# Optimization experiments

Hardware: AMD Instinct MI355X
Metric: run time of the kernel (lower is better)

Reference implementation:

```python
import jax, jax.numpy as jnp
import numpy as np

LN_EPS = 1e-5
LEAKY_SLOPE = 0.01


def setup_inputs() -> dict:
    key = jax.random.key(0)
    k1, k2, k3 = jax.random.split(key, 3)
    n, d, ns = 200000, 512, 1024
    x = jax.random.normal(k1, (n, d), dtype=jnp.float32)
    # Kaiming-ish scale for the projection weight [3d, d]
    W = jax.random.normal(k2, (3 * d, d), dtype=jnp.float32) * (1.0 / np.sqrt(3 * d))
    b = jnp.zeros((d,), dtype=jnp.float32)
    gamma = jnp.ones((d,), dtype=jnp.float32)
    beta = jnp.zeros((d,), dtype=jnp.float32)
    batch = jnp.sort(jax.random.randint(k3, (n,), 0, ns, dtype=jnp.int32))
    return {"x": x, "W": W, "b": b, "gamma": gamma, "beta": beta,
            "batch": batch, "num_segments": ns}


def _pool_mean_max_std(x, batch, num_segments):
    # single-pass style segment reductions: sum, sum-of-squares, count, max
    n = x.shape[0]
    count = jax.ops.segment_sum(jnp.ones((n,), x.dtype), batch, num_segments)  # [S]
    s = jax.ops.segment_sum(x, batch, num_segments)                            # [S,d]
    sq = jax.ops.segment_sum(x * x, batch, num_segments)                       # [S,d]
    cnt = jnp.maximum(count, 1.0)[:, None]
    mean = s / cnt                                                             # global_mean_pool
    # masked dense amax == segment max; empty segments -> finfo.min (NEG fill)
    NEG = jnp.finfo(x.dtype).min
    xmax = jax.ops.segment_max(x, batch, num_segments)
    xmax = jnp.where(jnp.isfinite(xmax), xmax, NEG)
    # scatter_std, unbiased=True, divisor clamped to >= 1 (torch_scatter semantics)
    var = (sq - mean * s) / jnp.maximum(count - 1.0, 1.0)[:, None]
    var = jnp.maximum(var, 0.0)
    safe = jnp.where(var > 0, var, 1.0)
    std = jnp.where(var > 0, jnp.sqrt(safe), 0.0)
    return jnp.concatenate([mean, xmax, std], axis=-1)  # [S, 3d]


def reference(x, W, b, gamma, beta, batch, num_segments):
    pooled = _pool_mean_max_std(x, batch, num_segments)        # [S, 3d]
    h = pooled @ W + b                                          # Linear
    mu = jnp.mean(h, axis=-1, keepdims=True)                    # LayerNorm (eps=1e-5)
    v = jnp.mean((h - mu) ** 2, axis=-1, keepdims=True)
    h = (h - mu) / jnp.sqrt(v + LN_EPS) * gamma + beta
    return jnp.where(h >= 0, h, LEAKY_SLOPE * h)                # LeakyReLU
```

## Files before the change

kernel.cpp:

```cpp
#include <hip/hip_runtime.h>
#include <math.h>

#define D 512
#define K3D 1536
#define NEGF (-3.40282346638528859812e+38f)

typedef __bf16 bf16x8 __attribute__((ext_vector_type(8)));
typedef unsigned short ushort8v __attribute__((ext_vector_type(8)));
typedef float f32x4 __attribute__((ext_vector_type(4)));

__device__ __forceinline__ unsigned short f2bf(float f) {
    unsigned int u = __float_as_uint(f);
    unsigned int r = (u + 0x7FFFu + ((u >> 16) & 1u)) >> 16;
    return (unsigned short)r;
}

__device__ __forceinline__ int lower_bound_dev(const int* __restrict__ b, int n, int v) {
    int lo = 0, hi = n;
    while (lo < hi) {
        int mid = (lo + hi) >> 1;
        if (b[mid] < v) lo = mid + 1; else hi = mid;
    }
    return lo;
}

__device__ __forceinline__ void acc4(float4& s, float4& q, float4& m, const float4 v) {
    s.x += v.x; s.y += v.y; s.z += v.z; s.w += v.w;
    q.x = fmaf(v.x, v.x, q.x); q.y = fmaf(v.y, v.y, q.y);
    q.z = fmaf(v.z, v.z, q.z); q.w = fmaf(v.w, v.w, q.w);
    m.x = fmaxf(m.x, v.x); m.y = fmaxf(m.y, v.y);
    m.z = fmaxf(m.z, v.z); m.w = fmaxf(m.w, v.w);
}

__global__ __launch_bounds__(512) void pool_kernel(
    const float* __restrict__ x, const int* __restrict__ batch,
    unsigned short* __restrict__ pooled_b, int n) {
    const int s   = blockIdx.x;
    const int col = threadIdx.x & 127;
    const int rg  = threadIdx.x >> 7;
    const int start = lower_bound_dev(batch, n, s);
    const int end   = lower_bound_dev(batch, n, s + 1);

    const float4* __restrict__ xv = (const float4*)x;

    float4 sum = {0.f, 0.f, 0.f, 0.f};
    float4 sq  = {0.f, 0.f, 0.f, 0.f};
    float4 mx  = {-INFINITY, -INFINITY, -INFINITY, -INFINITY};

    int i = start + rg;
    for (; i + 12 < end; i += 16) {
        float4 v0 = xv[(size_t)(i + 0)  * 128 + col];
        float4 v1 = xv[(size_t)(i + 4)  * 128 + col];
        float4 v2 = xv[(size_t)(i + 8)  * 128 + col];
        float4 v3 = xv[(size_t)(i + 12) * 128 + col];
        acc4(sum, sq, mx, v0);
        acc4(sum, sq, mx, v1);
        acc4(sum, sq, mx, v2);
        acc4(sum, sq, mx, v3);
    }
    for (; i < end; i += 4) {
        float4 v0 = xv[(size_t)i * 128 + col];
        acc4(sum, sq, mx, v0);
    }

    __shared__ __align__(16) float4 red[9 * 128];
    if (rg > 0) {
        const int base = (rg - 1) * 384;
        red[base + col]       = sum;
        red[base + 128 + col] = sq;
        red[base + 256 + col] = mx;
    }
    __syncthreads();
    if (rg == 0) {
#pragma unroll
        for (int g = 0; g < 3; ++g) {
            const int base = g * 384;
            float4 s2 = red[base + col];
            float4 q2 = red[base + 128 + col];
            float4 m2 = red[base + 256 + col];
            sum.x += s2.x; sum.y += s2.y; sum.z += s2.z; sum.w += s2.w;
            sq.x  += q2.x; sq.y  += q2.y; sq.z  += q2.z; sq.w  += q2.w;
            mx.x = fmaxf(mx.x, m2.x); mx.y = fmaxf(mx.y, m2.y);
            mx.z = fmaxf(mx.z, m2.z); mx.w = fmaxf(mx.w, m2.w);
        }

        const float cnt  = (float)(end - start);
        const float inv  = 1.f / fmaxf(cnt, 1.f);
        const float dinv = 1.f / fmaxf(cnt - 1.f, 1.f);

        float4 mean, stdv;
        mean.x = sum.x * inv; mean.y = sum.y * inv;
        mean.z = sum.z * inv; mean.w = sum.w * inv;

        float vx = (sq.x - mean.x * sum.x) * dinv;
        float vy = (sq.y - mean.y * sum.y) * dinv;
        float vz = (sq.z - mean.z * sum.z) * dinv;
        float vw = (sq.w - mean.w * sum.w) * dinv;
        vx = fmaxf(vx, 0.f); vy = fmaxf(vy, 0.f);
        vz = fmaxf(vz, 0.f); vw = fmaxf(vw, 0.f);
        stdv.x = vx > 0.f ? sqrtf(vx) : 0.f;
        stdv.y = vy > 0.f ? sqrtf(vy) : 0.f;
        stdv.z = vz > 0.f ? sqrtf(vz) : 0.f;
        stdv.w = vw > 0.f ? sqrtf(vw) : 0.f;

        float mxx = isfinite(mx.x) ? mx.x : NEGF;
        float mxy = isfinite(mx.y) ? mx.y : NEGF;
        float mxz = isfinite(mx.z) ? mx.z : NEGF;
        float mxw = isfinite(mx.w) ? mx.w : NEGF;

        unsigned short* prow = pooled_b + (size_t)s * K3D;
        ushort4 om = { f2bf(mean.x), f2bf(mean.y), f2bf(mean.z), f2bf(mean.w) };
        ushort4 ox = { f2bf(mxx),    f2bf(mxy),    f2bf(mxz),    f2bf(mxw)    };
        ushort4 os = { f2bf(stdv.x), f2bf(stdv.y), f2bf(stdv.z), f2bf(stdv.w) };
        *(ushort4*)&prow[4 * col]        = om;
        *(ushort4*)&prow[512 + 4 * col]  = ox;
        *(ushort4*)&prow[1024 + 4 * col] = os;
    }
}

__global__ __launch_bounds__(256) void wconv_kernel(
    const float* __restrict__ W, unsigned short* __restrict__ Wt) {
    __shared__ float tile[32][33];
    const int c0 = blockIdx.x * 32;
    const int r0 = blockIdx.y * 32;
    const int t = threadIdx.x;
    const int r = t >> 3, c4 = (t & 7) * 4;
    float4 v = *(const float4*)&W[(size_t)(r0 + r) * D + c0 + c4];
    tile[r][c4 + 0] = v.x; tile[r][c4 + 1] = v.y;
    tile[r][c4 + 2] = v.z; tile[r][c4 + 3] = v.w;
    __syncthreads();
    const int nn = t >> 3, k4 = (t & 7) * 4;
    ushort4 o = { f2bf(tile[k4 + 0][nn]), f2bf(tile[k4 + 1][nn]),
                  f2bf(tile[k4 + 2][nn]), f2bf(tile[k4 + 3][nn]) };
    *(ushort4*)&Wt[(size_t)(c0 + nn) * K3D + r0 + k4] = o;
}

#define GBM 64
#define GBN 64
#define GBK 64
#define LDT 88
#define GSPLIT 4
#define GKC (K3D / GSPLIT)

__global__ __launch_bounds__(256) void mfma_gemm(
    const unsigned short* __restrict__ A,
    const unsigned short* __restrict__ B,
    float* __restrict__ Hp, int S) {
    __shared__ unsigned short As[GBM * LDT];
    __shared__ unsigned short Bs[GBN * LDT];

    const int tid  = threadIdx.x;
    const int wave = tid >> 6;
    const int lane = tid & 63;
    const int m0 = blockIdx.y * GBM;
    const int n0 = blockIdx.x * GBN;
    const int kb = blockIdx.z * GKC;
    const int wm = (wave & 1) * 32;
    const int wn = (wave >> 1) * 32;

    const int sr = tid >> 3;
    const int sc = (tid & 7) * 8;

    const int frow = lane & 15;
    const int fk   = (lane >> 4) * 8;

    f32x4 acc00 = {0.f, 0.f, 0.f, 0.f};
    f32x4 acc01 = {0.f, 0.f, 0.f, 0.f};
    f32x4 acc10 = {0.f, 0.f, 0.f, 0.f};
    f32x4 acc11 = {0.f, 0.f, 0.f, 0.f};

    for (int k0 = kb; k0 < kb + GKC; k0 += GBK) {
        ushort8v a0 = *(const ushort8v*)&A[(size_t)(m0 + sr)      * K3D + k0 + sc];
        ushort8v a1 = *(const ushort8v*)&A[(size_t)(m0 + sr + 32) * K3D + k0 + sc];
        ushort8v b0 = *(const ushort8v*)&B[(size_t)(n0 + sr)      * K3D + k0 + sc];
        ushort8v b1 = *(const ushort8v*)&B[(size_t)(n0 + sr + 32) * K3D + k0 + sc];
        __syncthreads();
        *(ushort8v*)&As[(sr)      * LDT + sc] = a0;
        *(ushort8v*)&As[(sr + 32) * LDT + sc] = a1;
        *(ushort8v*)&Bs[(sr)      * LDT + sc] = b0;
        *(ushort8v*)&Bs[(sr + 32) * LDT + sc] = b1;
        __syncthreads();

#pragma unroll
        for (int ks = 0; ks < GBK; ks += 32) {
            bf16x8 af0 = *(const bf16x8*)&As[(wm + frow)      * LDT + ks + fk];
            bf16x8 af1 = *(const bf16x8*)&As[(wm + 16 + frow) * LDT + ks + fk];
            bf16x8 bv0 = *(const bf16x8*)&Bs[(wn + frow)      * LDT + ks + fk];
            bf16x8 bv1 = *(const bf16x8*)&Bs[(wn + 16 + frow) * LDT + ks + fk];
            acc00 = __builtin_amdgcn_mfma_f32_16x16x32_bf16(af0, bv0, acc00, 0, 0, 0);
            acc01 = __builtin_amdgcn_mfma_f32_16x16x32_bf16(af0, bv1, acc01, 0, 0, 0);
            acc10 = __builtin_amdgcn_mfma_f32_16x16x32_bf16(af1, bv0, acc10, 0, 0, 0);
            acc11 = __builtin_amdgcn_mfma_f32_16x16x32_bf16(af1, bv1, acc11, 0, 0, 0);
        }
    }

    float* out = Hp + (size_t)blockIdx.z * S * D;
    const int orow = (lane >> 4) * 4;
    const int ocol = lane & 15;
#pragma unroll
    for (int r = 0; r < 4; ++r) {
        out[(size_t)(m0 + wm +      orow + r) * D + n0 + wn +      ocol] = acc00[r];
        out[(size_t)(m0 + wm +      orow + r) * D + n0 + wn + 16 + ocol] = acc01[r];
        out[(size_t)(m0 + wm + 16 + orow + r) * D + n0 + wn +      ocol] = acc10[r];
        out[(size_t)(m0 + wm + 16 + orow + r) * D + n0 + wn + 16 + ocol] = acc11[r];
    }
}

__global__ __launch_bounds__(128) void ln_kernel(
    const float* __restrict__ Hp, const float* __restrict__ bias,
    const float* __restrict__ gamma, const float* __restrict__ beta,
    float* __restrict__ out, int S) {
    const int row = blockIdx.x;
    const int tid = threadIdx.x;
    const size_t idx = (size_t)row * 128 + tid;
    const size_t stride = (size_t)S * 128;

    const float4* hp = (const float4*)Hp;
    float4 v0 = hp[idx];
    float4 v1 = hp[idx + stride];
    float4 v2 = hp[idx + 2 * stride];
    float4 v3 = hp[idx + 3 * stride];
    float4 bb = *(const float4*)&bias[4 * tid];
    float4 v;
    v.x = (v0.x + v1.x) + (v2.x + v3.x) + bb.x;
    v.y = (v0.y + v1.y) + (v2.y + v3.y) + bb.y;
    v.z = (v0.z + v1.z) + (v2.z + v3.z) + bb.z;
    v.w = (v0.w + v1.w) + (v2.w + v3.w) + bb.w;

    float s = v.x + v.y + v.z + v.w;
    float q = v.x * v.x + v.y * v.y + v.z * v.z + v.w * v.w;
#pragma unroll
    for (int off = 32; off > 0; off >>= 1) {
        s += __shfl_down(s, off);
        q += __shfl_down(q, off);
    }
    __shared__ float ls[2], lq[2];
    const int wave = tid >> 6, lane = tid & 63;
    if (lane == 0) { ls[wave] = s; lq[wave] = q; }
    __syncthreads();
    s = ls[0] + ls[1];
    q = lq[0] + lq[1];

    const float mu = s * (1.f / 512.f);
    float var = q * (1.f / 512.f) - mu * mu;
    var = fmaxf(var, 0.f);
    const float r = rsqrtf(var + 1e-5f);

    float4 g  = *(const float4*)&gamma[4 * tid];
    float4 bt = *(const float4*)&beta[4 * tid];
    float4 o;
    o.x = (v.x - mu) * r * g.x + bt.x;
    o.y = (v.y - mu) * r * g.y + bt.y;
    o.z = (v.z - mu) * r * g.z + bt.z;
    o.w = (v.w - mu) * r * g.w + bt.w;
    o.x = o.x >= 0.f ? o.x : 0.01f * o.x;
    o.y = o.y >= 0.f ? o.y : 0.01f * o.y;
    o.z = o.z >= 0.f ? o.z : 0.01f * o.z;
    o.w = o.w >= 0.f ? o.w : 0.01f * o.w;
    *(float4*)&out[(size_t)row * D + 4 * tid] = o;
}

extern "C" void kernel_launch(void* const* d_in, const int* in_sizes, int n_in,
                              void* d_out, int out_size, void* d_ws, size_t ws_size,
                              hipStream_t stream) {
    const float* x     = (const float*)d_in[0];
    const float* W     = (const float*)d_in[1];
    const float* b     = (const float*)d_in[2];
    const float* gamma = (const float*)d_in[3];
    const float* beta  = (const float*)d_in[4];
    const int*   batch = (const int*)d_in[5];
    const int n = in_sizes[5];
    const int S = out_size / D;

    char* ws = (char*)d_ws;
    unsigned short* pooled_b = (unsigned short*)ws;
    unsigned short* Wt       = (unsigned short*)(ws + (size_t)S * K3D * 2);
    float*          Hp       = (float*)(ws + (size_t)S * K3D * 2 + (size_t)D * K3D * 2);
    float* out = (float*)d_out;

    pool_kernel<<<S, 512, 0, stream>>>(x, batch, pooled_b, n);
    dim3 gw(D / 32, K3D / 32);
    wconv_kernel<<<gw, 256, 0, stream>>>(W, Wt);
    dim3 gg(D / GBN, S / GBM, GSPLIT);
    mfma_gemm<<<gg, 256, 0, stream>>>(pooled_b, Wt, Hp, S);
    ln_kernel<<<S, 128, 0, stream>>>(Hp, b, gamma, beta, out, S);
}
```

Baseline: 560.0 us.

## Fuse pooling with weight conversion and precompute segment bounds separately

Segment boundaries move into a small bounds kernel, so each pool block no longer runs two binary searches over the batch array. The pooling and W transpose/bf16 conversion are merged into one launch, with the extra blocks handling 64x32 weight tiles, removing one kernel launch and letting the two jobs overlap. Loads of x now use nontemporal hints to avoid polluting cache with streaming data. The cost is an extra small kernel launch and a larger shared-memory footprint per block from the added tile array.

```diff
diff --git a/kernel.cpp b/kernel.cpp
--- a/kernel.cpp
+++ b/kernel.cpp
@@ -24,115 +24,113 @@
     return lo;
 }
 
-__device__ __forceinline__ void acc4(float4& s, float4& q, float4& m, const float4 v) {
-    s.x += v.x; s.y += v.y; s.z += v.z; s.w += v.w;
-    q.x = fmaf(v.x, v.x, q.x); q.y = fmaf(v.y, v.y, q.y);
-    q.z = fmaf(v.z, v.z, q.z); q.w = fmaf(v.w, v.w, q.w);
-    m.x = fmaxf(m.x, v.x); m.y = fmaxf(m.y, v.y);
-    m.z = fmaxf(m.z, v.z); m.w = fmaxf(m.w, v.w);
-}
-
-__global__ __launch_bounds__(512) void pool_kernel(
-    const float* __restrict__ x, const int* __restrict__ batch,
-    unsigned short* __restrict__ pooled_b, int n) {
-    const int s   = blockIdx.x;
-    const int col = threadIdx.x & 127;
-    const int rg  = threadIdx.x >> 7;
-    const int start = lower_bound_dev(batch, n, s);
-    const int end   = lower_bound_dev(batch, n, s + 1);
-
-    const float4* __restrict__ xv = (const float4*)x;
-
-    float4 sum = {0.f, 0.f, 0.f, 0.f};
-    float4 sq  = {0.f, 0.f, 0.f, 0.f};
-    float4 mx  = {-INFINITY, -INFINITY, -INFINITY, -INFINITY};
-
-    int i = start + rg;
-    for (; i + 12 < end; i += 16) {
-        float4 v0 = xv[(size_t)(i + 0)  * 128 + col];
-        float4 v1 = xv[(size_t)(i + 4)  * 128 + col];
-        float4 v2 = xv[(size_t)(i + 8)  * 128 + col];
-        float4 v3 = xv[(size_t)(i + 12) * 128 + col];
-        acc4(sum, sq, mx, v0);
-        acc4(sum, sq, mx, v1);
-        acc4(sum, sq, mx, v2);
-        acc4(sum, sq, mx, v3);
-    }
-    for (; i < end; i += 4) {
-        float4 v0 = xv[(size_t)i * 128 + col];
-        acc4(sum, sq, mx, v0);
-    }
-
-    __shared__ __align__(16) float4 red[9 * 128];
-    if (rg > 0) {
-        const int base = (rg - 1) * 384;
-        red[base + col]       = sum;
-        red[base + 128 + col] = sq;
-        red[base + 256 + col] = mx;
-    }
-    __syncthreads();
-    if (rg == 0) {
-#pragma unroll
-        for (int g = 0; g < 3; ++g) {
-            const int base = g * 384;
-            float4 s2 = red[base + col];
-            float4 q2 = red[base + 128 + col];
-            float4 m2 = red[base + 256 + col];
-            sum.x += s2.x; sum.y += s2.y; sum.z += s2.z; sum.w += s2.w;
-            sq.x  += q2.x; sq.y  += q2.y; sq.z  += q2.z; sq.w  += q2.w;
-            mx.x = fmaxf(mx.x, m2.x); mx.y = fmaxf(mx.y, m2.y);
-            mx.z = fmaxf(mx.z, m2.z); mx.w = fmaxf(mx.w, m2.w);
-        }
-
-        const float cnt  = (float)(end - start);
-        const float inv  = 1.f / fmaxf(cnt, 1.f);
-        const float dinv = 1.f / fmaxf(cnt - 1.f, 1.f);
-
-        float4 mean, stdv;
-        mean.x = sum.x * inv; mean.y = sum.y * inv;
-        mean.z = sum.z * inv; mean.w = sum.w * inv;
-
-        float vx = (sq.x - mean.x * sum.x) * dinv;
-        float vy = (sq.y - mean.y * sum.y) * dinv;
-        float vz = (sq.z - mean.z * sum.z) * dinv;
-        float vw = (sq.w - mean.w * sum.w) * dinv;
-        vx = fmaxf(vx, 0.f); vy = fmaxf(vy, 0.f);
-        vz = fmaxf(vz, 0.f); vw = fmaxf(vw, 0.f);
-        stdv.x = vx > 0.f ? sqrtf(vx) : 0.f;
-        stdv.y = vy > 0.f ? sqrtf(vy) : 0.f;
-        stdv.z = vz > 0.f ? sqrtf(vz) : 0.f;
-        stdv.w = vw > 0.f ? sqrtf(vw) : 0.f;
-
-        float mxx = isfinite(mx.x) ? mx.x : NEGF;
-        float mxy = isfinite(mx.y) ? mx.y : NEGF;
-        float mxz = isfinite(mx.z) ? mx.z : NEGF;
-        float mxw = isfinite(mx.w) ? mx.w : NEGF;
-
-        unsigned short* prow = pooled_b + (size_t)s * K3D;
-        ushort4 om = { f2bf(mean.x), f2bf(mean.y), f2bf(mean.z), f2bf(mean.w) };
-        ushort4 ox = { f2bf(mxx),    f2bf(mxy),    f2bf(mxz),    f2bf(mxw)    };
-        ushort4 os = { f2bf(stdv.x), f2bf(stdv.y), f2bf(stdv.z), f2bf(stdv.w) };
-        *(ushort4*)&prow[4 * col]        = om;
-        *(ushort4*)&prow[512 + 4 * col]  = ox;
-        *(ushort4*)&prow[1024 + 4 * col] = os;
-    }
-}
-
-__global__ __launch_bounds__(256) void wconv_kernel(
-    const float* __restrict__ W, unsigned short* __restrict__ Wt) {
-    __shared__ float tile[32][33];
-    const int c0 = blockIdx.x * 32;
-    const int r0 = blockIdx.y * 32;
-    const int t = threadIdx.x;
-    const int r = t >> 3, c4 = (t & 7) * 4;
-    float4 v = *(const float4*)&W[(size_t)(r0 + r) * D + c0 + c4];
-    tile[r][c4 + 0] = v.x; tile[r][c4 + 1] = v.y;
-    tile[r][c4 + 2] = v.z; tile[r][c4 + 3] = v.w;
-    __syncthreads();
-    const int nn = t >> 3, k4 = (t & 7) * 4;
-    ushort4 o = { f2bf(tile[k4 + 0][nn]), f2bf(tile[k4 + 1][nn]),
-                  f2bf(tile[k4 + 2][nn]), f2bf(tile[k4 + 3][nn]) };
-    *(ushort4*)&Wt[(size_t)(c0 + nn) * K3D + r0 + k4] = o;
+__device__ __forceinline__ void acc4(f32x4& s, f32x4& q, f32x4& m, const f32x4 v) {
+    s[0] += v[0]; s[1] += v[1]; s[2] += v[2]; s[3] += v[3];
+    q[0] = fmaf(v[0], v[0], q[0]); q[1] = fmaf(v[1], v[1], q[1]);
+    q[2] = fmaf(v[2], v[2], q[2]); q[3] = fmaf(v[3], v[3], q[3]);
+    m[0] = fmaxf(m[0], v[0]); m[1] = fmaxf(m[1], v[1]);
+    m[2] = fmaxf(m[2], v[2]); m[3] = fmaxf(m[3], v[3]);
+}
+
+__global__ __launch_bounds__(256) void bounds_kernel(
+    const int* __restrict__ batch, int* __restrict__ bounds, int n, int S) {
+    const int s = blockIdx.x * 256 + threadIdx.x;
+    if (s <= S) bounds[s] = lower_bound_dev(batch, n, s);
+}
+
+__global__ __launch_bounds__(512) void pool_wconv_kernel(
+    const float* __restrict__ x, const int* __restrict__ bounds,
+    unsigned short* __restrict__ pooled_b,
+    const float* __restrict__ W, unsigned short* __restrict__ Wt, int S) {
+    __shared__ __align__(16) f32x4 red[9 * 128];
+    __shared__ float tile[64][33];
+
+    if ((int)blockIdx.x < S) {
+        const int s   = blockIdx.x;
+        const int col = threadIdx.x & 127;
+        const int rg  = threadIdx.x >> 7;
+        const int start = bounds[s];
+        const int end   = bounds[s + 1];
+
+        const f32x4* __restrict__ xv = (const f32x4*)x;
+
+        f32x4 sum = {0.f, 0.f, 0.f, 0.f};
+        f32x4 sq  = {0.f, 0.f, 0.f, 0.f};
+        f32x4 mx  = {-INFINITY, -INFINITY, -INFINITY, -INFINITY};
+
+        int i = start + rg;
+        for (; i + 12 < end; i += 16) {
+            f32x4 v0 = __builtin_nontemporal_load(&xv[(size_t)(i + 0)  * 128 + col]);
+            f32x4 v1 = __builtin_nontemporal_load(&xv[(size_t)(i + 4)  * 128 + col]);
+            f32x4 v2 = __builtin_nontemporal_load(&xv[(size_t)(i + 8)  * 128 + col]);
+            f32x4 v3 = __builtin_nontemporal_load(&xv[(size_t)(i + 12) * 128 + col]);
+            acc4(sum, sq, mx, v0);
+            acc4(sum, sq, mx, v1);
+            acc4(sum, sq, mx, v2);
+            acc4(sum, sq, mx, v3);
+        }
+        for (; i < end; i += 4) {
+            f32x4 v0 = __builtin_nontemporal_load(&xv[(size_t)i * 128 + col]);
+            acc4(sum, sq, mx, v0);
+        }
+
+        if (rg > 0) {
+            const int base = (rg - 1) * 384;
+            red[base + col]       = sum;
+            red[base + 128 + col] = sq;
+            red[base + 256 + col] = mx;
+        }
+        __syncthreads();
+        if (rg == 0) {
+#pragma unroll
+            for (int g = 0; g < 3; ++g) {
+                const int base = g * 384;
+                f32x4 s2 = red[base + col];
+                f32x4 q2 = red[base + 128 + col];
+                f32x4 m2 = red[base + 256 + col];
+                sum[0] += s2[0]; sum[1] += s2[1]; sum[2] += s2[2]; sum[3] += s2[3];
+                sq[0]  += q2[0]; sq[1]  += q2[1]; sq[2]  += q2[2]; sq[3]  += q2[3];
+                mx[0] = fmaxf(mx[0], m2[0]); mx[1] = fmaxf(mx[1], m2[1]);
+                mx[2] = fmaxf(mx[2], m2[2]); mx[3] = fmaxf(mx[3], m2[3]);
+            }
+
+            const float cnt  = (float)(end - start);
+            const float inv  = 1.f / fmaxf(cnt, 1.f);
+            const float dinv = 1.f / fmaxf(cnt - 1.f, 1.f);
+
+            float mean[4], stdv[4], mxo[4];
+#pragma unroll
+            for (int j = 0; j < 4; ++j) {
+                mean[j] = sum[j] * inv;
+                float v = (sq[j] - mean[j] * sum[j]) * dinv;
+                v = fmaxf(v, 0.f);
+                stdv[j] = v > 0.f ? sqrtf(v) : 0.f;
+                mxo[j]  = isfinite(mx[j]) ? mx[j] : NEGF;
+            }
+
+            unsigned short* prow = pooled_b + (size_t)s * K3D;
+            ushort4 om = { f2bf(mean[0]), f2bf(mean[1]), f2bf(mean[2]), f2bf(mean[3]) };
+            ushort4 ox = { f2bf(mxo[0]),  f2bf(mxo[1]),  f2bf(mxo[2]),  f2bf(mxo[3])  };
+            ushort4 os = { f2bf(stdv[0]), f2bf(stdv[1]), f2bf(stdv[2]), f2bf(stdv[3]) };
+            *(ushort4*)&prow[4 * col]        = om;
+            *(ushort4*)&prow[512 + 4 * col]  = ox;
+            *(ushort4*)&prow[1024 + 4 * col] = os;
+        }
+    } else {
+        const int bid = (int)blockIdx.x - S;
+        const int c0 = (bid & 15) * 32;
+        const int r0 = (bid >> 4) * 64;
+        const int t = threadIdx.x;
+        const int r = t >> 3, c4 = (t & 7) * 4;
+        float4 v = *(const float4*)&W[(size_t)(r0 + r) * D + c0 + c4];
+        tile[r][c4 + 0] = v.x; tile[r][c4 + 1] = v.y;
+        tile[r][c4 + 2] = v.z; tile[r][c4 + 3] = v.w;
+        __syncthreads();
+        const int nn = t >> 4, k4 = (t & 15) * 4;
+        ushort4 o = { f2bf(tile[k4 + 0][nn]), f2bf(tile[k4 + 1][nn]),
+                      f2bf(tile[k4 + 2][nn]), f2bf(tile[k4 + 3][nn]) };
+        *(ushort4*)&Wt[(size_t)(c0 + nn) * K3D + r0 + k4] = o;
+    }
 }
 
 #define GBM 64
@@ -276,11 +274,13 @@
     unsigned short* pooled_b = (unsigned short*)ws;
     unsigned short* Wt       = (unsigned short*)(ws + (size_t)S * K3D * 2);
     float*          Hp       = (float*)(ws + (size_t)S * K3D * 2 + (size_t)D * K3D * 2);
+    int*            bounds   = (int*)(ws + (size_t)S * K3D * 2 + (size_t)D * K3D * 2
+                                         + (size_t)GSPLIT * S * D * 4);
     float* out = (float*)d_out;
 
-    pool_kernel<<<S, 512, 0, stream>>>(x, batch, pooled_b, n);
-    dim3 gw(D / 32, K3D / 32);
-    wconv_kernel<<<gw, 256, 0, stream>>>(W, Wt);
+    bounds_kernel<<<(S + 1 + 255) / 256, 256, 0, stream>>>(batch, bounds, n, S);
+    pool_wconv_kernel<<<S + (K3D / 64) * (D / 32), 512, 0, stream>>>(
+        x, bounds, pooled_b, W, Wt, S);
     dim3 gg(D / GBN, S / GBM, GSPLIT);
     mfma_gemm<<<gg, 256, 0, stream>>>(pooled_b, Wt, Hp, S);
     ln_kernel<<<S, 128, 0, stream>>>(Hp, b, gamma, beta, out, S);
```

Result: faster. 530.6 us (-5.2%).
